# Kernel optimization log

Hardware: AMD Instinct MI355X
Metric: run time of the kernel (lower is better)

Reference implementation:

```python
import jax, jax.numpy as jnp
import numpy as np

H = 8        # num_heads
D = 64       # qkv_dim
E = 512      # embed_dim = H*D
MS = 16      # ms_hidden_dim


def setup_inputs() -> dict:
    key = jax.random.key(0)
    ks = jax.random.split(key, 12)
    b, r, c = 4, 512, 512
    row_emb = jax.random.normal(ks[0], (b, r, E), dtype=jnp.float32)
    col_emb = jax.random.normal(ks[1], (b, c, E), dtype=jnp.float32)
    cost_mat = jax.random.uniform(ks[2], (b, r, c), dtype=jnp.float32)
    attn_mask = jax.random.randint(ks[3], (b, H, r, c), 0, 2) > 0
    s = 1.0 / np.sqrt(E)
    Wq = jax.random.uniform(ks[4], (H * D, E), minval=-s, maxval=s)
    Wk = jax.random.uniform(ks[5], (H * D, E), minval=-s, maxval=s)
    Wv = jax.random.uniform(ks[6], (H * D, E), minval=-s, maxval=s)
    Wout = jax.random.uniform(ks[7], (E, E), minval=-s, maxval=s)
    m1 = np.sqrt(0.5)
    m2 = np.sqrt(1.0 / MS)
    Wmix1 = jax.random.uniform(ks[8], (H * MS, 2 * H), minval=-m1, maxval=m1)
    Wmix2 = jax.random.uniform(ks[9], (H, H * MS), minval=-m2, maxval=m2)
    return {"row_emb": row_emb, "col_emb": col_emb, "cost_mat": cost_mat,
            "attn_mask": attn_mask, "Wq": Wq, "Wk": Wk, "Wv": Wv,
            "Wmix1": Wmix1, "Wmix2": Wmix2, "Wout": Wout}


def reference(row_emb, col_emb, cost_mat, attn_mask, Wq, Wk, Wv, Wmix1, Wmix2, Wout):
    b, r, _ = row_emb.shape
    c = col_emb.shape[1]
    norm = 1.0 / jnp.sqrt(jnp.asarray(D, row_emb.dtype))
    # projections -> [b, h, s, d]
    q = (row_emb @ Wq.T).reshape(b, r, H, D).transpose(0, 2, 1, 3)
    k = (col_emb @ Wk.T).reshape(b, c, H, D).transpose(0, 2, 1, 3)
    v = (col_emb @ Wv.T).reshape(b, c, H, D).transpose(0, 2, 1, 3)
    dot = norm * jnp.einsum('bhrd,bhcd->bhrc', q, k)            # [b,h,r,c]
    cost = jnp.broadcast_to(cost_mat[:, None, :, :], dot.shape)  # [b,h,r,c]
    # stack then rearrange 'b h r c s -> b r c (h s)' (h major, s minor)
    two = jnp.stack([dot, cost], axis=-1)                        # [b,h,r,c,2]
    two = two.transpose(0, 2, 3, 1, 4).reshape(b, r, c, 2 * H)
    hid = jax.nn.relu(two @ Wmix1.T)                             # [b,r,c,H*MS]
    ms = hid @ Wmix2.T                                           # [b,r,c,H]
    logits = ms.transpose(0, 3, 1, 2)                            # [b,h,r,c]
    # mask handling: rows that are fully masked become fully unmasked
    all_masked = jnp.all(attn_mask, axis=-1, keepdims=True)
    mask = jnp.where(all_masked, False, attn_mask)
    logits = jnp.where(mask, -jnp.inf, logits)
    weights = jax.nn.softmax(logits, axis=-1)
    out = jnp.einsum('bhrc,bhcd->bhrd', weights, v)              # [b,h,r,d]
    out = out.transpose(0, 2, 1, 3).reshape(b, r, H * D)         # b s (h d)
    return out @ Wout.T
```

## Files before the change

kernel.cpp:

```cpp
#include <hip/hip_runtime.h>
#include <math.h>

typedef __attribute__((ext_vector_type(8))) short bf16x8;
typedef __attribute__((ext_vector_type(4))) float f32x4;
typedef __attribute__((ext_vector_type(8))) _Float16 f16x8_t;
typedef unsigned short ushort_t;

static __device__ inline unsigned short f2bf(float f) {
    union { float f; unsigned u; } v; v.f = f;
    unsigned r = v.u + 0x7fff + ((v.u >> 16) & 1);
    return (unsigned short)(r >> 16);
}

static __device__ inline unsigned pk2bf(float a, float b) {
    unsigned r;
    asm("v_cvt_pk_bf16_f32 %0, %1, %2" : "=v"(r) : "v"(a), "v"(b));
    return r;
}

__global__ __launch_bounds__(256) void convert_all(const float* __restrict__ a0,
                                                   const float* __restrict__ a1,
                                                   const float* __restrict__ a2,
                                                   const float* __restrict__ a3,
                                                   const float* __restrict__ a4,
                                                   const float* __restrict__ a5,
                                                   const float* __restrict__ W1,
                                                   const float* __restrict__ W2,
                                                   ushort_t* __restrict__ dst,
                                                   ushort_t* __restrict__ tab) {
    if (blockIdx.x >= 3072) {
        const int t = threadIdx.x;
        if (t < 64) {
            const int quad = t >> 4;
            const int sl   = t & 15;
#pragma unroll
            for (int nt = 0; nt < 8; ++nt) {
                union { ushort_t s[8]; uint4 u; } vv;
#pragma unroll
                for (int i = 0; i < 8; ++i) vv.s[i] = 0;
                if (quad < 2) {
                    const int j = nt * 16 + sl;
#pragma unroll
                    for (int i = 0; i < 8; ++i) {
                        const int k = quad * 8 + i;
                        if (k < 8) {
                            vv.s[i] = f2bf(W1[j * 16 + 2 * k]);
                        } else if (k == 8) {
                            float s = 0.f;
#pragma unroll
                            for (int h = 0; h < 8; ++h) s += W1[j * 16 + 2 * h + 1];
                            vv.s[i] = f2bf(s);
                        }
                    }
                }
                *(uint4*)(tab + (nt * 64 + t) * 8) = vv.u;
            }
#pragma unroll
            for (int ks = 0; ks < 4; ++ks) {
                union { ushort_t s[8]; uint4 u; } vv;
#pragma unroll
                for (int i = 0; i < 8; ++i) {
                    const int j = (2 * ks + (i >> 2)) * 16 + quad * 4 + (i & 3);
                    vv.s[i] = (sl < 8) ? f2bf(W2[sl * 128 + j]) : (ushort_t)0;
                }
                *(uint4*)(tab + 4096 + (ks * 64 + t) * 8) = vv.u;
            }
        }
        return;
    }

    const size_t e = ((size_t)blockIdx.x * 256 + threadIdx.x) * 4;
    const float* src; size_t off;
    if      (e < 1048576) { src = a0; off = 0; }
    else if (e < 2097152) { src = a1; off = 1048576; }
    else if (e < 2359296) { src = a2; off = 2097152; }
    else if (e < 2621440) { src = a3; off = 2359296; }
    else if (e < 2883584) { src = a4; off = 2621440; }
    else                  { src = a5; off = 2883584; }
    const float4 v = *(const float4*)(src + (e - off));
    uint2 o; o.x = pk2bf(v.x, v.y); o.y = pk2bf(v.z, v.w);
    *(uint2*)(dst + e) = o;
}

__global__ __launch_bounds__(256) void gemm_qkv(const ushort_t* __restrict__ rowb,
                                                const ushort_t* __restrict__ colb,
                                                const ushort_t* __restrict__ Wqb,
                                                const ushort_t* __restrict__ Wkb,
                                                const ushort_t* __restrict__ Wvb,
                                                ushort_t* __restrict__ Qb,
                                                ushort_t* __restrict__ Kb,
                                                ushort_t* __restrict__ Vt) {
    const int z = blockIdx.z;
    const ushort_t* A = (z == 0) ? rowb : colb;
    const ushort_t* B = (z == 0) ? Wqb : (z == 1) ? Wkb : Wvb;

    const int t    = threadIdx.x;
    const int w    = t >> 6;
    const int lane = t & 63;
    const int quad = lane >> 4;
    const int sl   = lane & 15;
    const int m0 = blockIdx.x * 64 + (w >> 1) * 32;
    const int n0 = blockIdx.y * 64 + (w & 1) * 32;

    f32x4 acc[2][2] = {};

    for (int k0 = 0; k0 < 512; k0 += 32) {
        bf16x8 a[2], b[2];
#pragma unroll
        for (int rs = 0; rs < 2; ++rs)
            a[rs] = *(const bf16x8*)(A + (size_t)(m0 + rs * 16 + sl) * 512 + k0 + quad * 8);
#pragma unroll
        for (int cs = 0; cs < 2; ++cs)
            b[cs] = *(const bf16x8*)(B + (size_t)(n0 + cs * 16 + sl) * 512 + k0 + quad * 8);
#pragma unroll
        for (int rs = 0; rs < 2; ++rs)
#pragma unroll
            for (int cs = 0; cs < 2; ++cs)
                acc[rs][cs] = __builtin_amdgcn_mfma_f32_16x16x32_bf16(a[rs], b[cs], acc[rs][cs], 0, 0, 0);
    }

#pragma unroll
    for (int rs = 0; rs < 2; ++rs)
#pragma unroll
        for (int cs = 0; cs < 2; ++cs) {
            const int n = n0 + cs * 16 + sl;
            if (z == 2) {
                const int mb   = m0 + rs * 16 + quad * 4;
                const int bidx = mb >> 9, c = mb & 511;
                const int h = n >> 6, d = n & 63;
                uint2 o;
                o.x = pk2bf(acc[rs][cs][0], acc[rs][cs][1]);
                o.y = pk2bf(acc[rs][cs][2], acc[rs][cs][3]);
                *(uint2*)(Vt + (size_t)(((bidx * 8 + h) * 64 + d)) * 512 + c) = o;
            } else {
                ushort_t* C = (z == 0) ? Qb : Kb;
#pragma unroll
                for (int reg = 0; reg < 4; ++reg) {
                    const int m = m0 + rs * 16 + quad * 4 + reg;
                    C[(size_t)m * 512 + n] = f2bf(acc[rs][cs][reg]);
                }
            }
        }
}

__global__ __launch_bounds__(256) void gemm_out(const ushort_t* __restrict__ A,
                                                const ushort_t* __restrict__ B,
                                                float* __restrict__ C) {
    const int t    = threadIdx.x;
    const int w    = t >> 6;
    const int lane = t & 63;
    const int quad = lane >> 4;
    const int sl   = lane & 15;
    const int m0 = blockIdx.x * 64 + (w >> 1) * 32;
    const int n0 = blockIdx.y * 64 + (w & 1) * 32;

    f32x4 acc[2][2] = {};

    for (int k0 = 0; k0 < 512; k0 += 32) {
        bf16x8 a[2], b[2];
#pragma unroll
        for (int rs = 0; rs < 2; ++rs)
            a[rs] = *(const bf16x8*)(A + (size_t)(m0 + rs * 16 + sl) * 512 + k0 + quad * 8);
#pragma unroll
        for (int cs = 0; cs < 2; ++cs)
            b[cs] = *(const bf16x8*)(B + (size_t)(n0 + cs * 16 + sl) * 512 + k0 + quad * 8);
#pragma unroll
        for (int rs = 0; rs < 2; ++rs)
#pragma unroll
            for (int cs = 0; cs < 2; ++cs)
                acc[rs][cs] = __builtin_amdgcn_mfma_f32_16x16x32_bf16(a[rs], b[cs], acc[rs][cs], 0, 0, 0);
    }

#pragma unroll
    for (int rs = 0; rs < 2; ++rs)
#pragma unroll
        for (int cs = 0; cs < 2; ++cs) {
            const int n = n0 + cs * 16 + sl;
#pragma unroll
            for (int reg = 0; reg < 4; ++reg) {
                const int m = m0 + rs * 16 + quad * 4 + reg;
                C[(size_t)m * 512 + n] = acc[rs][cs][reg];
            }
        }
}

__global__ __launch_bounds__(256) void dot_mlp_v9(const ushort_t* __restrict__ Qb,
                                                  const ushort_t* __restrict__ Kb,
                                                  const float* __restrict__ cost,
                                                  const ushort_t* __restrict__ tab,
                                                  _Float16* __restrict__ logits) {
    __shared__ ushort_t Xs[512 * 20];

    const int b  = blockIdx.z;
    const int r0 = blockIdx.y * 32;
    const int c0 = blockIdx.x * 16;
    const int t    = threadIdx.x;
    const int w    = t >> 6;
    const int lane = t & 63;
    const int quad = lane >> 4;
    const int sl   = lane & 15;

#pragma unroll
    for (int i = 0; i < 2; ++i) {
        const int cell = t + i * 256;
        const int rl = cell >> 4, cl = cell & 15;
        unsigned* base = (unsigned*)(Xs + cell * 20) + 4;
        base[0] = (unsigned)f2bf(cost[((size_t)b * 512 + r0 + rl) * 512 + c0 + cl]);
        base[1] = 0; base[2] = 0; base[3] = 0;
    }

    bf16x8 aw1[8], w2f[4];
#pragma unroll
    for (int nt = 0; nt < 8; ++nt)
        aw1[nt] = *(const bf16x8*)(tab + (nt * 64 + lane) * 8);
#pragma unroll
    for (int ks = 0; ks < 4; ++ks)
        w2f[ks] = *(const bf16x8*)(tab + 4096 + (ks * 64 + lane) * 8);

    {
        const int rs  = w >> 1;
        const int hbj = w & 1;
        unsigned uu[2][4];
#pragma unroll
        for (int hp = 0; hp < 2; ++hp) {
            const int h0 = hbj * 4 + hp * 2;
            bf16x8 qa[2][2], ka[2][2];
#pragma unroll
            for (int hh = 0; hh < 2; ++hh)
#pragma unroll
                for (int ks = 0; ks < 2; ++ks) {
                    qa[hh][ks] = *(const bf16x8*)(Qb +
                        ((size_t)(b * 512 + r0 + rs * 16 + sl) * 512 + (h0 + hh) * 64 + ks * 32 + quad * 8));
                    ka[hh][ks] = *(const bf16x8*)(Kb +
                        ((size_t)(b * 512 + c0 + sl) * 512 + (h0 + hh) * 64 + ks * 32 + quad * 8));
                }
            f32x4 ac0 = {0.f, 0.f, 0.f, 0.f}, ac1 = {0.f, 0.f, 0.f, 0.f};
            ac0 = __builtin_amdgcn_mfma_f32_16x16x32_bf16(qa[0][0], ka[0][0], ac0, 0, 0, 0);
            ac0 = __builtin_amdgcn_mfma_f32_16x16x32_bf16(qa[0][1], ka[0][1], ac0, 0, 0, 0);
            ac1 = __builtin_amdgcn_mfma_f32_16x16x32_bf16(qa[1][0], ka[1][0], ac1, 0, 0, 0);
            ac1 = __builtin_amdgcn_mfma_f32_16x16x32_bf16(qa[1][1], ka[1][1], ac1, 0, 0, 0);
#pragma unroll
            for (int reg = 0; reg < 4; ++reg)
                uu[hp][reg] = pk2bf(ac0[reg] * 0.125f, ac1[reg] * 0.125f);
        }
        const int rowb = rs * 16 + quad * 4;
#pragma unroll
        for (int reg = 0; reg < 4; ++reg) {
            const int cell = (rowb + reg) * 16 + sl;
            unsigned* xp = (unsigned*)(Xs + cell * 20) + hbj * 2;
            xp[0] = uu[0][reg];
            xp[1] = uu[1][reg];
        }
    }

    __syncthreads();

    const bf16x8 zf = {0, 0, 0, 0, 0, 0, 0, 0};
#pragma unroll
    for (int mt = 0; mt < 8; ++mt) {
        const int gmt  = w * 8 + mt;
        const int cell = gmt * 16 + sl;

        bf16x8 a1 = zf;
        if (quad < 2) {
            const unsigned* xr = (const unsigned*)Xs + (size_t)cell * 10 + quad * 4;
            union { unsigned u[4]; bf16x8 v; } tmp;
            tmp.u[0] = xr[0]; tmp.u[1] = xr[1]; tmp.u[2] = xr[2]; tmp.u[3] = xr[3];
            a1 = tmp.v;
        }

        f32x4 acc2 = {0.f, 0.f, 0.f, 0.f};
#pragma unroll
        for (int ks = 0; ks < 4; ++ks) {
            f32x4 z = {0.f, 0.f, 0.f, 0.f};
            const f32x4 h0v = __builtin_amdgcn_mfma_f32_16x16x32_bf16(aw1[2 * ks],     a1, z, 0, 0, 0);
            const f32x4 h1v = __builtin_amdgcn_mfma_f32_16x16x32_bf16(aw1[2 * ks + 1], a1, z, 0, 0, 0);
            union { unsigned u[4]; bf16x8 v; } hb;
            hb.u[0] = pk2bf(fmaxf(h0v[0], 0.f), fmaxf(h0v[1], 0.f));
            hb.u[1] = pk2bf(fmaxf(h0v[2], 0.f), fmaxf(h0v[3], 0.f));
            hb.u[2] = pk2bf(fmaxf(h1v[0], 0.f), fmaxf(h1v[1], 0.f));
            hb.u[3] = pk2bf(fmaxf(h1v[2], 0.f), fmaxf(h1v[3], 0.f));
            acc2 = __builtin_amdgcn_mfma_f32_16x16x32_bf16(w2f[ks], hb.v, acc2, 0, 0, 0);
        }

        if (quad < 2) {
            const int r = r0 + gmt;
            const int c = c0 + sl;
#pragma unroll
            for (int reg = 0; reg < 4; ++reg) {
                const int h = quad * 4 + reg;
                logits[((size_t)(b * 8 + h) * 512 + r) * 512 + c] = (_Float16)acc2[reg];
            }
        }
    }
}

__global__ __launch_bounds__(256) void softmax_pv(const _Float16* __restrict__ logits,
                                                  const int* __restrict__ mask,
                                                  const ushort_t* __restrict__ Vt,
                                                  ushort_t* __restrict__ Aout) {
    __shared__ ushort_t Ps[32 * 522];

    const int t    = threadIdx.x;
    const int w    = t >> 6;
    const int lane = t & 63;
    const int quad = lane >> 4;
    const int sl   = lane & 15;
    const int rt = blockIdx.x;
    const int bh = blockIdx.y;
    const int r0 = rt * 32;

#pragma unroll
    for (int rr = 0; rr < 8; ++rr) {
        const int row = w * 8 + rr;
        const _Float16* lp = logits + ((size_t)bh * 512 + r0 + row) * 512;
        const int*      mp = mask   + ((size_t)bh * 512 + r0 + row) * 512;

        const f16x8_t fv = ((const f16x8_t*)lp)[lane];
        const int4    m0 = ((const int4*)mp)[2 * lane];
        const int4    m1 = ((const int4*)mp)[2 * lane + 1];

        float v[8]; int m[8];
#pragma unroll
        for (int i = 0; i < 8; ++i) v[i] = (float)fv[i];
        m[0] = m0.x; m[1] = m0.y; m[2] = m0.z; m[3] = m0.w;
        m[4] = m1.x; m[5] = m1.y; m[6] = m1.z; m[7] = m1.w;

        int allm = 1;
#pragma unroll
        for (int i = 0; i < 8; ++i) allm &= (m[i] != 0);
        const bool all_masked = (__all(allm) != 0);

        float mx = -__builtin_inff();
#pragma unroll
        for (int i = 0; i < 8; ++i) {
            const bool keep = all_masked || (m[i] == 0);
            if (keep) mx = fmaxf(mx, v[i]);
        }
#pragma unroll
        for (int s = 32; s > 0; s >>= 1) mx = fmaxf(mx, __shfl_xor(mx, s, 64));

        float e[8]; float sum = 0.f;
#pragma unroll
        for (int i = 0; i < 8; ++i) {
            const bool keep = all_masked || (m[i] == 0);
            e[i] = keep ? __expf(v[i] - mx) : 0.f;
            sum += e[i];
        }
#pragma unroll
        for (int s = 32; s > 0; s >>= 1) sum += __shfl_xor(sum, s, 64);

        const float inv = 1.f / sum;
        unsigned* pr = (unsigned*)Ps + 261 * row + 4 * lane;
        pr[0] = pk2bf(e[0] * inv, e[1] * inv);
        pr[1] = pk2bf(e[2] * inv, e[3] * inv);
        pr[2] = pk2bf(e[4] * inv, e[5] * inv);
        pr[3] = pk2bf(e[6] * inv, e[7] * inv);
    }

    __syncthreads();

    const int mt  = w >> 1;
    const int n0w = (w & 1) * 32;
    const ushort_t* vb = Vt + (size_t)bh * 64 * 512;

    f32x4 acc[2] = {};
#pragma unroll 4
    for (int ks = 0; ks < 16; ++ks) {
        union { unsigned u[4]; bf16x8 v; } ta;
        const ushort_t* pp = Ps + (size_t)(mt * 16 + sl) * 522 + ks * 32 + quad * 8;
        ta.u[0] = *(const unsigned*)(pp);
        ta.u[1] = *(const unsigned*)(pp + 2);
        ta.u[2] = *(const unsigned*)(pp + 4);
        ta.u[3] = *(const unsigned*)(pp + 6);
        bf16x8 bv[2];
#pragma unroll
        for (int cn = 0; cn < 2; ++cn)
            bv[cn] = *(const bf16x8*)(vb + (size_t)(n0w + cn * 16 + sl) * 512 + ks * 32 + quad * 8);
#pragma unroll
        for (int cn = 0; cn < 2; ++cn)
            acc[cn] = __builtin_amdgcn_mfma_f32_16x16x32_bf16(ta.v, bv[cn], acc[cn], 0, 0, 0);
    }

    const int bidx = bh >> 3, h = bh & 7;
    ushort_t* Cb = Aout + (size_t)bidx * 512 * 512 + h * 64;
#pragma unroll
    for (int cn = 0; cn < 2; ++cn) {
        const int n = n0w + cn * 16 + sl;
#pragma unroll
        for (int reg = 0; reg < 4; ++reg) {
            const int m = r0 + mt * 16 + quad * 4 + reg;
            Cb[(size_t)m * 512 + n] = f2bf(acc[cn][reg]);
        }
    }
}

extern "C" void kernel_launch(void* const* d_in, const int* in_sizes, int n_in,
                              void* d_out, int out_size, void* d_ws, size_t ws_size,
                              hipStream_t stream) {
    const float* row_emb = (const float*)d_in[0];
    const float* col_emb = (const float*)d_in[1];
    const float* cost    = (const float*)d_in[2];
    const int*   mask    = (const int*)d_in[3];
    const float* Wq      = (const float*)d_in[4];
    const float* Wk      = (const float*)d_in[5];
    const float* Wv      = (const float*)d_in[6];
    const float* Wmix1   = (const float*)d_in[7];
    const float* Wmix2   = (const float*)d_in[8];
    const float* Wout    = (const float*)d_in[9];
    float* out = (float*)d_out;

    char* ws = (char*)d_ws;
    const size_t MB = (size_t)1 << 20;
    ushort_t* convDst = (ushort_t*)ws;
    ushort_t* rowb  = (ushort_t*)(ws);
    ushort_t* colb  = (ushort_t*)(ws + 2 * MB);
    ushort_t* Wqb   = (ushort_t*)(ws + 4 * MB);
    ushort_t* Wkb   = (ushort_t*)(ws + 4 * MB + 512 * 1024);
    ushort_t* Wvb   = (ushort_t*)(ws + 5 * MB);
    ushort_t* Woutb = (ushort_t*)(ws + 5 * MB + 512 * 1024);
    ushort_t* Qb    = (ushort_t*)(ws + 6 * MB);
    ushort_t* Kb    = (ushort_t*)(ws + 8 * MB);
    ushort_t* Vt    = (ushort_t*)(ws + 10 * MB);
    ushort_t* Aoutb = (ushort_t*)(ws + 12 * MB);
    ushort_t* fragTab = (ushort_t*)(ws + 14 * MB);
    _Float16* logitsBuf = (_Float16*)(ws + 40 * MB);

    convert_all<<<3073, 256, 0, stream>>>(row_emb, col_emb, Wq, Wk, Wv, Wout,
                                          Wmix1, Wmix2, convDst, fragTab);

    gemm_qkv<<<dim3(32, 8, 3), 256, 0, stream>>>(rowb, colb, Wqb, Wkb, Wvb, Qb, Kb, Vt);

    dot_mlp_v9<<<dim3(32, 16, 4), 256, 0, stream>>>(Qb, Kb, cost, fragTab, logitsBuf);

    softmax_pv<<<dim3(16, 32), 256, 0, stream>>>(logitsBuf, mask, Vt, Aoutb);

    gemm_out<<<dim3(32, 8), 256, 0, stream>>>(Aoutb, Woutb, out);
}
```

Before: 186.4 us.

## Process four column tiles per block with double-buffered K and cost prefetch

The dot+MLP kernel now handles 64 columns per block in four 16-column steps instead of one. Q fragments and the MLP weight fragments are loaded once and reused across those steps. K fragments and cost values for the next step are prefetched into registers while the current step runs. The grid shrinks fourfold and each step adds an extra barrier. The two GEMM k-loops also get unroll-by-2 hints, and register pressure rises from the doubled K buffers.

```diff
diff --git a/kernel.cpp b/kernel.cpp
--- a/kernel.cpp
+++ b/kernel.cpp
@@ -104,6 +104,7 @@
 
     f32x4 acc[2][2] = {};
 
+#pragma unroll 2
     for (int k0 = 0; k0 < 512; k0 += 32) {
         bf16x8 a[2], b[2];
 #pragma unroll
@@ -156,6 +157,7 @@
 
     f32x4 acc[2][2] = {};
 
+#pragma unroll 2
     for (int k0 = 0; k0 < 512; k0 += 32) {
         bf16x8 a[2], b[2];
 #pragma unroll
@@ -184,29 +186,29 @@
         }
 }
 
-__global__ __launch_bounds__(256) void dot_mlp_v9(const ushort_t* __restrict__ Qb,
-                                                  const ushort_t* __restrict__ Kb,
-                                                  const float* __restrict__ cost,
-                                                  const ushort_t* __restrict__ tab,
-                                                  _Float16* __restrict__ logits) {
+__global__ __launch_bounds__(256) void dot_mlp_v10(const ushort_t* __restrict__ Qb,
+                                                   const ushort_t* __restrict__ Kb,
+                                                   const float* __restrict__ cost,
+                                                   const ushort_t* __restrict__ tab,
+                                                   _Float16* __restrict__ logits) {
     __shared__ ushort_t Xs[512 * 20];
 
     const int b  = blockIdx.z;
     const int r0 = blockIdx.y * 32;
-    const int c0 = blockIdx.x * 16;
+    const int cb = blockIdx.x * 64;
     const int t    = threadIdx.x;
     const int w    = t >> 6;
     const int lane = t & 63;
     const int quad = lane >> 4;
     const int sl   = lane & 15;
+    const int rs  = w >> 1;
+    const int hbj = w & 1;
 
 #pragma unroll
     for (int i = 0; i < 2; ++i) {
         const int cell = t + i * 256;
-        const int rl = cell >> 4, cl = cell & 15;
-        unsigned* base = (unsigned*)(Xs + cell * 20) + 4;
-        base[0] = (unsigned)f2bf(cost[((size_t)b * 512 + r0 + rl) * 512 + c0 + cl]);
-        base[1] = 0; base[2] = 0; base[3] = 0;
+        unsigned* base = (unsigned*)(Xs + cell * 20) + 5;
+        base[0] = 0; base[1] = 0; base[2] = 0;
     }
 
     bf16x8 aw1[8], w2f[4];
@@ -217,82 +219,123 @@
     for (int ks = 0; ks < 4; ++ks)
         w2f[ks] = *(const bf16x8*)(tab + 4096 + (ks * 64 + lane) * 8);
 
-    {
-        const int rs  = w >> 1;
-        const int hbj = w & 1;
-        unsigned uu[2][4];
-#pragma unroll
-        for (int hp = 0; hp < 2; ++hp) {
-            const int h0 = hbj * 4 + hp * 2;
-            bf16x8 qa[2][2], ka[2][2];
-#pragma unroll
-            for (int hh = 0; hh < 2; ++hh)
-#pragma unroll
-                for (int ks = 0; ks < 2; ++ks) {
-                    qa[hh][ks] = *(const bf16x8*)(Qb +
-                        ((size_t)(b * 512 + r0 + rs * 16 + sl) * 512 + (h0 + hh) * 64 + ks * 32 + quad * 8));
-                    ka[hh][ks] = *(const bf16x8*)(Kb +
-                        ((size_t)(b * 512 + c0 + sl) * 512 + (h0 + hh) * 64 + ks * 32 + quad * 8));
+    bf16x8 qa[2][2][2];
+#pragma unroll
+    for (int hp = 0; hp < 2; ++hp)
+#pragma unroll
+        for (int hh = 0; hh < 2; ++hh)
+#pragma unroll
+            for (int ks = 0; ks < 2; ++ks)
+                qa[hp][hh][ks] = *(const bf16x8*)(Qb +
+                    ((size_t)(b * 512 + r0 + rs * 16 + sl) * 512 +
+                     (hbj * 4 + hp * 2 + hh) * 64 + ks * 32 + quad * 8));
+
+    bf16x8 ka[2][2][2][2];
+    float  cpre[2][2];
+
+#define LOAD_KC(ci, buf)                                                        \
+    {                                                                           \
+        const int c0_ = cb + (ci) * 16;                                         \
+        _Pragma("unroll")                                                       \
+        for (int hp = 0; hp < 2; ++hp)                                          \
+            _Pragma("unroll")                                                   \
+            for (int hh = 0; hh < 2; ++hh)                                      \
+                _Pragma("unroll")                                               \
+                for (int ks = 0; ks < 2; ++ks)                                  \
+                    ka[buf][hp][hh][ks] = *(const bf16x8*)(Kb +                 \
+                        ((size_t)(b * 512 + c0_ + sl) * 512 +                   \
+                         (hbj * 4 + hp * 2 + hh) * 64 + ks * 32 + quad * 8));   \
+        _Pragma("unroll")                                                       \
+        for (int i = 0; i < 2; ++i) {                                           \
+            const int cell_ = t + i * 256;                                      \
+            const int rl_ = cell_ >> 4, cl_ = cell_ & 15;                       \
+            cpre[buf][i] = cost[((size_t)b * 512 + r0 + rl_) * 512 + c0_ + cl_];\
+        }                                                                       \
+    }
+
+    LOAD_KC(0, 0);
+
+    const bf16x8 zf = {0, 0, 0, 0, 0, 0, 0, 0};
+
+#pragma unroll
+    for (int ci = 0; ci < 4; ++ci) {
+        const int buf = ci & 1;
+        const int c0  = cb + ci * 16;
+
+#pragma unroll
+        for (int i = 0; i < 2; ++i) {
+            const int cell = t + i * 256;
+            *((unsigned*)(Xs + cell * 20) + 4) = (unsigned)f2bf(cpre[buf][i]);
+        }
+
+        {
+            unsigned uu[2][4];
+#pragma unroll
+            for (int hp = 0; hp < 2; ++hp) {
+                f32x4 ac0 = {0.f, 0.f, 0.f, 0.f}, ac1 = {0.f, 0.f, 0.f, 0.f};
+                ac0 = __builtin_amdgcn_mfma_f32_16x16x32_bf16(qa[hp][0][0], ka[buf][hp][0][0], ac0, 0, 0, 0);
+                ac0 = __builtin_amdgcn_mfma_f32_16x16x32_bf16(qa[hp][0][1], ka[buf][hp][0][1], ac0, 0, 0, 0);
+                ac1 = __builtin_amdgcn_mfma_f32_16x16x32_bf16(qa[hp][1][0], ka[buf][hp][1][0], ac1, 0, 0, 0);
+                ac1 = __builtin_amdgcn_mfma_f32_16x16x32_bf16(qa[hp][1][1], ka[buf][hp][1][1], ac1, 0, 0, 0);
+#pragma unroll
+                for (int reg = 0; reg < 4; ++reg)
+                    uu[hp][reg] = pk2bf(ac0[reg] * 0.125f, ac1[reg] * 0.125f);
+            }
+            const int rowb = rs * 16 + quad * 4;
+#pragma unroll
+            for (int reg = 0; reg < 4; ++reg) {
+                const int cell = (rowb + reg) * 16 + sl;
+                unsigned* xp = (unsigned*)(Xs + cell * 20) + hbj * 2;
+                xp[0] = uu[0][reg];
+                xp[1] = uu[1][reg];
+            }
+        }
+
+        if (ci < 3) LOAD_KC(ci + 1, buf ^ 1);
+
+        __syncthreads();
+
+#pragma unroll
+        for (int mt = 0; mt < 8; ++mt) {
+            const int gmt  = w * 8 + mt;
+            const int cell = gmt * 16 + sl;
+
+            bf16x8 a1 = zf;
+            if (quad < 2) {
+                const unsigned* xr = (const unsigned*)Xs + (size_t)cell * 10 + quad * 4;
+                union { unsigned u[4]; bf16x8 v; } tmp;
+                tmp.u[0] = xr[0]; tmp.u[1] = xr[1]; tmp.u[2] = xr[2]; tmp.u[3] = xr[3];
+                a1 = tmp.v;
+            }
+
+            f32x4 acc2 = {0.f, 0.f, 0.f, 0.f};
+#pragma unroll
+            for (int ks = 0; ks < 4; ++ks) {
+                f32x4 z = {0.f, 0.f, 0.f, 0.f};
+                const f32x4 h0v = __builtin_amdgcn_mfma_f32_16x16x32_bf16(aw1[2 * ks],     a1, z, 0, 0, 0);
+                const f32x4 h1v = __builtin_amdgcn_mfma_f32_16x16x32_bf16(aw1[2 * ks + 1], a1, z, 0, 0, 0);
+                union { unsigned u[4]; bf16x8 v; } hb;
+                hb.u[0] = pk2bf(fmaxf(h0v[0], 0.f), fmaxf(h0v[1], 0.f));
+                hb.u[1] = pk2bf(fmaxf(h0v[2], 0.f), fmaxf(h0v[3], 0.f));
+                hb.u[2] = pk2bf(fmaxf(h1v[0], 0.f), fmaxf(h1v[1], 0.f));
+                hb.u[3] = pk2bf(fmaxf(h1v[2], 0.f), fmaxf(h1v[3], 0.f));
+                acc2 = __builtin_amdgcn_mfma_f32_16x16x32_bf16(w2f[ks], hb.v, acc2, 0, 0, 0);
+            }
+
+            if (quad < 2) {
+                const int r = r0 + gmt;
+                const int c = c0 + sl;
+#pragma unroll
+                for (int reg = 0; reg < 4; ++reg) {
+                    const int h = quad * 4 + reg;
+                    logits[((size_t)(b * 8 + h) * 512 + r) * 512 + c] = (_Float16)acc2[reg];
                 }
-            f32x4 ac0 = {0.f, 0.f, 0.f, 0.f}, ac1 = {0.f, 0.f, 0.f, 0.f};
-            ac0 = __builtin_amdgcn_mfma_f32_16x16x32_bf16(qa[0][0], ka[0][0], ac0, 0, 0, 0);
-            ac0 = __builtin_amdgcn_mfma_f32_16x16x32_bf16(qa[0][1], ka[0][1], ac0, 0, 0, 0);
-            ac1 = __builtin_amdgcn_mfma_f32_16x16x32_bf16(qa[1][0], ka[1][0], ac1, 0, 0, 0);
-            ac1 = __builtin_amdgcn_mfma_f32_16x16x32_bf16(qa[1][1], ka[1][1], ac1, 0, 0, 0);
-#pragma unroll
-            for (int reg = 0; reg < 4; ++reg)
-                uu[hp][reg] = pk2bf(ac0[reg] * 0.125f, ac1[reg] * 0.125f);
-        }
-        const int rowb = rs * 16 + quad * 4;
-#pragma unroll
-        for (int reg = 0; reg < 4; ++reg) {
-            const int cell = (rowb + reg) * 16 + sl;
-            unsigned* xp = (unsigned*)(Xs + cell * 20) + hbj * 2;
-            xp[0] = uu[0][reg];
-            xp[1] = uu[1][reg];
-        }
-    }
-
-    __syncthreads();
-
-    const bf16x8 zf = {0, 0, 0, 0, 0, 0, 0, 0};
-#pragma unroll
-    for (int mt = 0; mt < 8; ++mt) {
-        const int gmt  = w * 8 + mt;
-        const int cell = gmt * 16 + sl;
-
-        bf16x8 a1 = zf;
-        if (quad < 2) {
-            const unsigned* xr = (const unsigned*)Xs + (size_t)cell * 10 + quad * 4;
-            union { unsigned u[4]; bf16x8 v; } tmp;
-            tmp.u[0] = xr[0]; tmp.u[1] = xr[1]; tmp.u[2] = xr[2]; tmp.u[3] = xr[3];
-            a1 = tmp.v;
-        }
-
-        f32x4 acc2 = {0.f, 0.f, 0.f, 0.f};
-#pragma unroll
-        for (int ks = 0; ks < 4; ++ks) {
-            f32x4 z = {0.f, 0.f, 0.f, 0.f};
-            const f32x4 h0v = __builtin_amdgcn_mfma_f32_16x16x32_bf16(aw1[2 * ks],     a1, z, 0, 0, 0);
-            const f32x4 h1v = __builtin_amdgcn_mfma_f32_16x16x32_bf16(aw1[2 * ks + 1], a1, z, 0, 0, 0);
-            union { unsigned u[4]; bf16x8 v; } hb;
-            hb.u[0] = pk2bf(fmaxf(h0v[0], 0.f), fmaxf(h0v[1], 0.f));
-            hb.u[1] = pk2bf(fmaxf(h0v[2], 0.f), fmaxf(h0v[3], 0.f));
-            hb.u[2] = pk2bf(fmaxf(h1v[0], 0.f), fmaxf(h1v[1], 0.f));
-            hb.u[3] = pk2bf(fmaxf(h1v[2], 0.f), fmaxf(h1v[3], 0.f));
-            acc2 = __builtin_amdgcn_mfma_f32_16x16x32_bf16(w2f[ks], hb.v, acc2, 0, 0, 0);
-        }
-
-        if (quad < 2) {
-            const int r = r0 + gmt;
-            const int c = c0 + sl;
-#pragma unroll
-            for (int reg = 0; reg < 4; ++reg) {
-                const int h = quad * 4 + reg;
-                logits[((size_t)(b * 8 + h) * 512 + r) * 512 + c] = (_Float16)acc2[reg];
-            }
-        }
-    }
+            }
+        }
+
+        __syncthreads();
+    }
+#undef LOAD_KC
 }
 
 __global__ __launch_bounds__(256) void softmax_pv(const _Float16* __restrict__ logits,
@@ -431,7 +474,7 @@
 
     gemm_qkv<<<dim3(32, 8, 3), 256, 0, stream>>>(rowb, colb, Wqb, Wkb, Wvb, Qb, Kb, Vt);
 
-    dot_mlp_v9<<<dim3(32, 16, 4), 256, 0, stream>>>(Qb, Kb, cost, fragTab, logitsBuf);
+    dot_mlp_v10<<<dim3(8, 16, 4), 256, 0, stream>>>(Qb, Kb, cost, fragTab, logitsBuf);
 
     softmax_pv<<<dim3(16, 32), 256, 0, stream>>>(logitsBuf, mask, Vt, Aoutb);
 
```

Result: no change. 187.4 us (+0.5%).
